# Kernel optimization log

Measured on AMD Instinct MI355X. Metric: run time of the kernel, lower is better.

## Reference

```python
import jax, jax.numpy as jnp
import numpy as np
from jax import lax

B, H, W, C = 8, 128, 128, 192
NUM_HEADS = 4
EPS = 1e-12  # tf.nn.l2_normalize epsilon


def _l2_normalize(x, axis=-1):
    sq = jnp.sum(x * x, axis=axis, keepdims=True)
    return x * lax.rsqrt(jnp.maximum(sq, EPS))


def setup_inputs() -> dict:
    key = jax.random.key(0)
    k1, k2, k3, k4 = jax.random.split(key, 4)
    x = jax.random.normal(k1, (B, H, W, C), dtype=jnp.float32)
    # 1x1 conv -> stored as [C, 3C] matrix
    qkv_w = jax.random.normal(k2, (C, 3 * C), dtype=jnp.float32) * 0.05
    # depthwise 3x3 conv, groups = 3C: HWIO kernel with I=1, O=3C
    dw_w = jax.random.normal(k3, (3, 3, 1, 3 * C), dtype=jnp.float32) * 0.05
    # 1x1 projection conv -> [C, C]
    proj_w = jax.random.normal(k4, (C, C), dtype=jnp.float32) * 0.05
    temperature = jnp.ones((NUM_HEADS, 1, 1), dtype=jnp.float32)
    return {"x": x, "qkv_w": qkv_w, "dw_w": dw_w, "proj_w": proj_w,
            "temperature": temperature}


def reference(x, qkv_w, dw_w, proj_w, temperature):
    b, h, w, c = x.shape
    heads = NUM_HEADS
    c_head = c // heads
    hw = h * w

    # 1x1 conv (no bias)
    qkv = jnp.einsum('bhwc,cd->bhwd', x, qkv_w)  # [b,h,w,3c]
    # depthwise 3x3 conv, SAME padding, groups = 3c
    qkv = lax.conv_general_dilated(
        qkv, dw_w, window_strides=(1, 1), padding='SAME',
        dimension_numbers=('NHWC', 'HWIO', 'NHWC'),
        feature_group_count=3 * c)

    q, k, v = jnp.split(qkv, 3, axis=-1)  # each [b,h,w,c]
    # faithful raw row-major reshape as in the TF code
    q = q.reshape(b, heads, c_head, hw)
    k = k.reshape(b, heads, c_head, hw)
    v = v.reshape(b, heads, c_head, hw)

    q = _l2_normalize(q, axis=-1)
    k = _l2_normalize(k, axis=-1)

    # channel-wise (transposed) attention: [b,heads,c_head,c_head]
    attn = jnp.einsum('bncs,bnds->bncd', q, k)
    attn = attn * temperature[None]  # temperature: [heads,1,1]
    attn = jax.nn.softmax(attn, axis=-1)

    out = jnp.einsum('bncd,bnds->bncs', attn, v)  # [b,heads,c_head,hw]
    out = out.reshape(b, h, w, c)
    out = jnp.einsum('bhwc,cd->bhwd', out, proj_w)  # 1x1 projection
    return out
```

## Files before the change

kernel.cpp:

```cpp
#include <hip/hip_runtime.h>
#include <math.h>

#define HWP 16384
#define CIN 192
#define C3  576
#define CH  48
#define NHD 4
#define NS  32
#define PBF 3145728
#define KG  192

typedef unsigned short u16;
typedef __attribute__((ext_vector_type(8))) short bf16x8;
typedef __attribute__((ext_vector_type(4))) float f32x4;

__device__ __forceinline__ u16 f2bf(float f) {
  unsigned int u = __builtin_bit_cast(unsigned int, f);
  u = (u + 0x7FFFu + ((u >> 16) & 1u)) >> 16;
  return (u16)u;
}
__device__ __forceinline__ float bflo(unsigned int u) {
  return __builtin_bit_cast(float, u << 16);
}
__device__ __forceinline__ float bfhi(unsigned int u) {
  return __builtin_bit_cast(float, u & 0xFFFF0000u);
}
__device__ __forceinline__ unsigned pk2(float a, float b) {
  return (unsigned)f2bf(a) | ((unsigned)f2bf(b) << 16);
}

__device__ __forceinline__ void gload16(const u16* g, u16* l) {
  __builtin_amdgcn_global_load_lds(
      (const __attribute__((address_space(1))) void*)g,
      (__attribute__((address_space(3))) void*)l, 16, 0, 0);
}

__global__ __launch_bounds__(256) void convert_x_k(
    const float* __restrict__ in, u16* __restrict__ out) {
  size_t base = ((size_t)blockIdx.x * 256 + threadIdx.x) * 8;
  float4 a = *(const float4*)&in[base];
  float4 b = *(const float4*)&in[base + 4];
  uint4 o;
  o.x = pk2(a.x, a.y); o.y = pk2(a.z, a.w);
  o.z = pk2(b.x, b.y); o.w = pk2(b.z, b.w);
  *(uint4*)&out[base] = o;
}

__global__ __launch_bounds__(256) void convert_w_k(
    const float* __restrict__ qkvW, const float* __restrict__ projW,
    u16* __restrict__ qkvWT, u16* __restrict__ projWT) {
  int idx = blockIdx.x * 256 + threadIdx.x;
  if (idx < C3 * CIN) {
    int n = idx / CIN, k = idx % CIN;
    qkvWT[idx] = f2bf(qkvW[(size_t)k * C3 + n]);
  } else {
    int i2 = idx - C3 * CIN;
    if (i2 < CIN * CIN) {
      int n = i2 / CIN, k = i2 % CIN;
      projWT[i2] = f2bf(projW[(size_t)k * CIN + n]);
    }
  }
}

template <bool C_BF16>
__global__ __launch_bounds__(256) void gemm1(
    const u16* __restrict__ A, const u16* __restrict__ BT, void* __restrict__ Cv,
    int N) {
  __shared__ __align__(16) u16 As[128 * KG];
  __shared__ __align__(16) u16 Bs[64 * KG];
  const int t = threadIdx.x;
  const int lane = t & 63, wave = t >> 6;
  const int nT = N >> 6;
  const int nwg = gridDim.x;
  const int bid = blockIdx.x;
  const int q = nwg >> 3, r = nwg & 7;
  const int xcd = bid & 7, idx = bid >> 3;
  const int swz = (xcd < r) ? (xcd * (q + 1) + idx)
                            : (r * (q + 1) + (xcd - r) * q + idx);
  const int m0 = (swz / nT) * 128, n0 = (swz % nT) * 64;
  const int wm = (wave >> 1) * 64, wn = (wave & 1) * 32;
  const int wbase = wave * 64;

#pragma unroll
  for (int i = 0; i < 12; ++i) {
    int slot = i * 256 + t;
    int row = slot / 24, c = slot % 24;
    int g = (c & ~7) | ((c & 7) ^ (row & 7));
    gload16(A + (size_t)(m0 + row) * KG + g * 8, As + (size_t)(i * 256 + wbase) * 8);
  }
#pragma unroll
  for (int i = 0; i < 6; ++i) {
    int slot = i * 256 + t;
    int row = slot / 24, c = slot % 24;
    int g = (c & ~7) | ((c & 7) ^ (row & 7));
    gload16(BT + (size_t)(n0 + row) * KG + g * 8, Bs + (size_t)(i * 256 + wbase) * 8);
  }
  __syncthreads();

  f32x4 acc[4][2];
#pragma unroll
  for (int mi = 0; mi < 4; ++mi)
#pragma unroll
    for (int ni = 0; ni < 2; ++ni) acc[mi][ni] = (f32x4){0.f, 0.f, 0.f, 0.f};

  const int lrow = lane & 15;
  const int lg16 = (lane >> 4) * 16;
#pragma unroll
  for (int kk = 0; kk < 6; ++kk) {
    const int colb = kk * 64 + lg16;
    bf16x8 a[4], b[2];
#pragma unroll
    for (int mi = 0; mi < 4; ++mi) {
      int row = wm + mi * 16 + lrow;
      a[mi] = *(const bf16x8*)((char*)As + row * 384 + (colb ^ ((row & 7) << 4)));
    }
#pragma unroll
    for (int ni = 0; ni < 2; ++ni) {
      int row = wn + ni * 16 + lrow;
      b[ni] = *(const bf16x8*)((char*)Bs + row * 384 + (colb ^ ((row & 7) << 4)));
    }
#pragma unroll
    for (int mi = 0; mi < 4; ++mi)
#pragma unroll
      for (int ni = 0; ni < 2; ++ni)
        acc[mi][ni] = __builtin_amdgcn_mfma_f32_16x16x32_bf16(a[mi], b[ni], acc[mi][ni], 0, 0, 0);
  }

  const int crow = (lane >> 4) * 4, ccol = lane & 15;
#pragma unroll
  for (int mi = 0; mi < 4; ++mi)
#pragma unroll
    for (int ni = 0; ni < 2; ++ni)
#pragma unroll
      for (int rr = 0; rr < 4; ++rr) {
        size_t off = (size_t)(m0 + wm + mi * 16 + crow + rr) * N + n0 + wn + ni * 16 + ccol;
        if (C_BF16) ((u16*)Cv)[off] = f2bf(acc[mi][ni][rr]);
        else        ((float*)Cv)[off] = acc[mi][ni][rr];
      }
}

__global__ __launch_bounds__(192) void dwconv_k(
    const u16* __restrict__ pre, const float* __restrict__ dwW,
    u16* __restrict__ qb, u16* __restrict__ kb, u16* __restrict__ vb,
    float* __restrict__ psum, int b0) {
  __shared__ __align__(16) u16 lds[2400 * 8];
  const int t = threadIdx.x;
  const int tile = blockIdx.x, sel = blockIdx.y, brel = blockIdx.z;
  const int h0 = (tile >> 4) * 8, w0 = (tile & 15) * 8;
  const int cg = t % 24, tw = t / 24;
  const int c = sel * 192 + cg * 8;

  float wgt[9][8];
#pragma unroll
  for (int tap = 0; tap < 9; ++tap) {
    float4 a = *(const float4*)&dwW[(size_t)tap * C3 + c];
    float4 b = *(const float4*)&dwW[(size_t)tap * C3 + c + 4];
    wgt[tap][0] = a.x; wgt[tap][1] = a.y; wgt[tap][2] = a.z; wgt[tap][3] = a.w;
    wgt[tap][4] = b.x; wgt[tap][5] = b.y; wgt[tap][6] = b.z; wgt[tap][7] = b.w;
  }

  const u16* src = pre + (size_t)brel * HWP * C3;
#pragma unroll
  for (int r = 0; r < 13; ++r) {
    int slot = t + r * 192;
    if (slot < 2400) {
      int pix = r * 8 + tw;
      int py = pix / 10, px = pix % 10;
      int gh = h0 - 1 + py, gw = w0 - 1 + px;
      uint4 v = make_uint4(0, 0, 0, 0);
      if ((unsigned)gh < 128u && (unsigned)gw < 128u)
        v = *(const uint4*)&src[(size_t)((gh << 7) + gw) * C3 + c];
      *(uint4*)&lds[slot * 8] = v;
    }
  }
  __syncthreads();

  float ssum[8] = {};
  u16* dstb = (sel == 0 ? qb : sel == 1 ? kb : vb) + (size_t)brel * PBF;
#pragma unroll
  for (int r = 0; r < 8; ++r) {
    float acc[8] = {};
#pragma unroll
    for (int dy = 0; dy < 3; ++dy)
#pragma unroll
      for (int dx = 0; dx < 3; ++dx) {
        uint4 v = *(const uint4*)&lds[(((r + dy) * 10 + tw + dx) * 24 + cg) * 8];
        const float* wg = wgt[dy * 3 + dx];
        acc[0] += bflo(v.x) * wg[0]; acc[1] += bfhi(v.x) * wg[1];
        acc[2] += bflo(v.y) * wg[2]; acc[3] += bfhi(v.y) * wg[3];
        acc[4] += bflo(v.z) * wg[4]; acc[5] += bfhi(v.z) * wg[5];
        acc[6] += bflo(v.w) * wg[6]; acc[7] += bfhi(v.w) * wg[7];
      }
    uint4 o;
    o.x = pk2(acc[0], acc[1]); o.y = pk2(acc[2], acc[3]);
    o.z = pk2(acc[4], acc[5]); o.w = pk2(acc[6], acc[7]);
    *(uint4*)&dstb[(size_t)(((h0 + r) << 7) + w0 + tw) * CIN + cg * 8] = o;
    if (sel < 2) {
#pragma unroll
      for (int i = 0; i < 8; ++i) ssum[i] += acc[i] * acc[i];
    }
  }

  if (sel < 2) {
    __syncthreads();
    float* fl = (float*)lds;
#pragma unroll
    for (int i = 0; i < 8; ++i) fl[tw * 192 + cg * 8 + i] = ssum[i];
    __syncthreads();
    float s = 0.f;
#pragma unroll
    for (int tw2 = 0; tw2 < 8; ++tw2) s += fl[tw2 * 192 + t];
    psum[(((size_t)sel * 8 + (b0 + brel)) * 192 + t) * 256 + tile] = s;
  }
}

__global__ __launch_bounds__(192) void rownorm2_k(
    const float* __restrict__ psum, float* __restrict__ rq, float* __restrict__ rk,
    int b0) {
  int sel = blockIdx.x, brel = blockIdx.y;
  int b = b0 + brel;
  int t = threadIdx.x;
  const float* p = psum + (((size_t)sel * 8 + b) * 192 + t) * 256;
  float s = 0.f;
#pragma unroll 4
  for (int i = 0; i < 256; i += 4) {
    float4 v = *(const float4*)&p[i];
    s += v.x + v.y + v.z + v.w;
  }
  (sel ? rk : rq)[b * CIN + t] = rsqrtf(fmaxf(s, 1e-12f));
}

__global__ __launch_bounds__(64) void qk_mfma_k(
    const u16* __restrict__ qbuf, const u16* __restrict__ kbuf,
    float* __restrict__ partial, int b0) {
  int sc = blockIdx.x, n = blockIdx.y, brel = blockIdx.z;
  int b = b0 + brel;
  const int lane = threadIdx.x;
  const u16* qp = qbuf + (size_t)brel * PBF + (size_t)n * CH * HWP;
  const u16* kp = kbuf + (size_t)brel * PBF + (size_t)n * CH * HWP;
  const int lrow = lane & 15;
  const int lko = (lane >> 4) * 8;
  f32x4 acc[3][3];
#pragma unroll
  for (int mi = 0; mi < 3; ++mi)
#pragma unroll
    for (int nj = 0; nj < 3; ++nj) acc[mi][nj] = (f32x4){0.f, 0.f, 0.f, 0.f};

  const int sBeg = sc * 512;
#pragma unroll 4
  for (int kk = 0; kk < 16; ++kk) {
    const int s0 = sBeg + kk * 32 + lko;
    bf16x8 a[3], bb[3];
#pragma unroll
    for (int mi = 0; mi < 3; ++mi)
      a[mi] = *(const bf16x8*)&qp[(size_t)(mi * 16 + lrow) * HWP + s0];
#pragma unroll
    for (int nj = 0; nj < 3; ++nj)
      bb[nj] = *(const bf16x8*)&kp[(size_t)(nj * 16 + lrow) * HWP + s0];
#pragma unroll
    for (int mi = 0; mi < 3; ++mi)
#pragma unroll
      for (int nj = 0; nj < 3; ++nj)
        acc[mi][nj] = __builtin_amdgcn_mfma_f32_16x16x32_bf16(a[mi], bb[nj], acc[mi][nj], 0, 0, 0);
  }

  const int crow = (lane >> 4) * 4, ccol = lane & 15;
  float* pout = partial + (((size_t)b * NHD + n) * NS + sc) * CH * CH;
#pragma unroll
  for (int mi = 0; mi < 3; ++mi)
#pragma unroll
    for (int nj = 0; nj < 3; ++nj)
#pragma unroll
      for (int rr = 0; rr < 4; ++rr)
        pout[(size_t)(mi * 16 + crow + rr) * CH + nj * 16 + ccol] = acc[mi][nj][rr];
}

__global__ __launch_bounds__(64) void softmax_k(
    const float* __restrict__ partial, const float* __restrict__ rq, const float* __restrict__ rk,
    const float* __restrict__ temp, float* __restrict__ attn, int b0) {
  int i = blockIdx.x % CH;
  int n = (blockIdx.x / CH) % NHD;
  int brel = blockIdx.x / (CH * NHD);
  int b = b0 + brel;
  int j = threadIdx.x;
  float logit = -INFINITY;
  if (j < CH) {
    float s = 0.f;
#pragma unroll 8
    for (int sc = 0; sc < NS; ++sc)
      s += partial[((((size_t)b * NHD + n) * NS + sc) * CH + i) * CH + j];
    logit = s * rq[b * CIN + n * CH + i] * rk[b * CIN + n * CH + j] * temp[n];
  }
  float m = logit;
#pragma unroll
  for (int o = 32; o > 0; o >>= 1) m = fmaxf(m, __shfl_xor(m, o));
  float e = (j < CH) ? expf(logit - m) : 0.f;
  float sum = e;
#pragma unroll
  for (int o = 32; o > 0; o >>= 1) sum += __shfl_xor(sum, o);
  if (j < CH) attn[(((size_t)b * NHD + n) * CH + i) * CH + j] = e / sum;
}

__global__ __launch_bounds__(256) void av_k(
    const float* __restrict__ attn, const u16* __restrict__ vbuf,
    u16* __restrict__ obuf, int b0) {
  int st = blockIdx.x, n = blockIdx.y, brel = blockIdx.z;
  int b = b0 + brel;
  __shared__ float as_[CH * CH];
  int t = threadIdx.x;
  const float* ap = attn + ((size_t)b * NHD + n) * CH * CH;
#pragma unroll
  for (int r = 0; r < 9; ++r) as_[t + r * 256] = ap[t + r * 256];
  __syncthreads();
  int s = st * 512 + t * 2;
  const u16* vp = vbuf + (size_t)brel * PBF + (size_t)n * CH * HWP;
  float2 acc[CH];
#pragma unroll
  for (int d = 0; d < CH; ++d) { acc[d].x = 0.f; acc[d].y = 0.f; }
#pragma unroll 4
  for (int j4 = 0; j4 < 12; ++j4) {
    unsigned int u0 = *(const unsigned int*)&vp[(size_t)(j4 * 4 + 0) * HWP + s];
    unsigned int u1 = *(const unsigned int*)&vp[(size_t)(j4 * 4 + 1) * HWP + s];
    unsigned int u2 = *(const unsigned int*)&vp[(size_t)(j4 * 4 + 2) * HWP + s];
    unsigned int u3 = *(const unsigned int*)&vp[(size_t)(j4 * 4 + 3) * HWP + s];
    float2 v0 = make_float2(bflo(u0), bfhi(u0));
    float2 v1 = make_float2(bflo(u1), bfhi(u1));
    float2 v2 = make_float2(bflo(u2), bfhi(u2));
    float2 v3 = make_float2(bflo(u3), bfhi(u3));
#pragma unroll
    for (int d = 0; d < CH; ++d) {
      float4 a4 = *(const float4*)&as_[d * CH + j4 * 4];
      acc[d].x += a4.x * v0.x + a4.y * v1.x + a4.z * v2.x + a4.w * v3.x;
      acc[d].y += a4.x * v0.y + a4.y * v1.y + a4.z * v2.y + a4.w * v3.y;
    }
  }
  u16* op = obuf + (size_t)brel * PBF + (size_t)n * CH * HWP;
#pragma unroll
  for (int d = 0; d < CH; ++d) {
    ushort2 o; o.x = f2bf(acc[d].x); o.y = f2bf(acc[d].y);
    *(ushort2*)&op[(size_t)d * HWP + s] = o;
  }
}

extern "C" void kernel_launch(void* const* d_in, const int* in_sizes, int n_in,
                              void* d_out, int out_size, void* d_ws, size_t ws_size,
                              hipStream_t stream) {
  const float* x      = (const float*)d_in[0];
  const float* qkv_w  = (const float*)d_in[1];
  const float* dw_w   = (const float*)d_in[2];
  const float* proj_w = (const float*)d_in[3];
  const float* temp   = (const float*)d_in[4];
  float* out = (float*)d_out;

  float* rq      = (float*)d_ws;
  float* rk      = rq + 8 * CIN;
  float* attn    = rk + 8 * CIN;
  float* partial = attn + 8 * NHD * CH * CH;
  float* psum    = partial + (size_t)8 * NHD * NS * CH * CH;
  u16* qkvwT  = (u16*)(psum + (size_t)2 * 8 * 192 * 256);
  u16* projwT = qkvwT + (size_t)C3 * CIN;
  u16* xbf    = projwT + (size_t)CIN * CIN;
  char* bufbase = (char*)(xbf + (size_t)8 * HWP * CIN);
  size_t off = (size_t)(bufbase - (char*)d_ws);
  off = (off + 255) & ~(size_t)255;

  const size_t perBatchBytes = (size_t)HWP * C3 * 2 + 4 * (size_t)PBF * 2;
  size_t avail = ws_size > off ? ws_size - off : 0;
  int nb = (int)(avail / perBatchBytes);
  if (nb < 1) nb = 1;
  if (nb > 8) nb = 8;

  u16* qkv_pre = (u16*)((char*)d_ws + off);
  u16* qbuf = qkv_pre + (size_t)nb * HWP * C3;
  u16* kbuf = qbuf + (size_t)nb * PBF;
  u16* vbuf = kbuf + (size_t)nb * PBF;
  u16* obuf = vbuf + (size_t)nb * PBF;

  convert_x_k<<<dim3((8 * HWP * CIN) / 2048), 256, 0, stream>>>(x, xbf);
  convert_w_k<<<dim3((C3 * CIN + CIN * CIN + 255) / 256), 256, 0, stream>>>(
      qkv_w, proj_w, qkvwT, projwT);

  for (int b0 = 0; b0 < 8; b0 += nb) {
    int nbc = (8 - b0) < nb ? (8 - b0) : nb;
    int M = nbc * HWP;
    gemm1<true><<<dim3((M / 128) * (C3 / 64)), 256, 0, stream>>>(
        xbf + (size_t)b0 * HWP * CIN, qkvwT, qkv_pre, C3);
    dwconv_k<<<dim3(256, 3, nbc), 192, 0, stream>>>(
        qkv_pre, dw_w, qbuf, kbuf, vbuf, psum, b0);
    rownorm2_k<<<dim3(2, nbc), 192, 0, stream>>>(psum, rq, rk, b0);
    qk_mfma_k<<<dim3(NS, NHD, nbc), 64, 0, stream>>>(qbuf, kbuf, partial, b0);
    softmax_k<<<dim3(nbc * NHD * CH), 64, 0, stream>>>(partial, rq, rk, temp, attn, b0);
    av_k<<<dim3(HWP / 512, NHD, nbc), 256, 0, stream>>>(attn, vbuf, obuf, b0);
    gemm1<false><<<dim3((M / 128) * (CIN / 64)), 256, 0, stream>>>(
        obuf, projwT, out + (size_t)b0 * HWP * CIN, CIN);
  }
}
```

Baseline: 382.5 us.

## Make GEMM persistent over M tiles with double-buffered A loads

The one-shot 128x64 GEMM kernel is replaced by one where each workgroup keeps its 64-column B tile resident in LDS and walks eight 64-row A tiles. The next A tile is prefetched into a second LDS buffer while the current one is computed. This cuts repeated B loads and launch and prologue overhead per tile, and overlaps global loads with MFMA work. In exchange the grid has fewer workgroups, each wave does less MFMA work per tile, and a barrier is added every iteration.

```diff
diff --git a/kernel.cpp b/kernel.cpp
--- a/kernel.cpp
+++ b/kernel.cpp
@@ -9,6 +9,7 @@
 #define NS  32
 #define PBF 3145728
 #define KG  192
+#define MT  8
 
 typedef unsigned short u16;
 typedef __attribute__((ext_vector_type(8))) short bf16x8;
@@ -63,31 +64,23 @@
 }
 
 template <bool C_BF16>
-__global__ __launch_bounds__(256) void gemm1(
+__global__ __launch_bounds__(256) void gemm2(
     const u16* __restrict__ A, const u16* __restrict__ BT, void* __restrict__ Cv,
     int N) {
-  __shared__ __align__(16) u16 As[128 * KG];
   __shared__ __align__(16) u16 Bs[64 * KG];
+  __shared__ __align__(16) u16 As[2][64 * KG];
   const int t = threadIdx.x;
   const int lane = t & 63, wave = t >> 6;
   const int nT = N >> 6;
-  const int nwg = gridDim.x;
-  const int bid = blockIdx.x;
+  const int nwg = gridDim.x, bid = blockIdx.x;
   const int q = nwg >> 3, r = nwg & 7;
   const int xcd = bid & 7, idx = bid >> 3;
   const int swz = (xcd < r) ? (xcd * (q + 1) + idx)
                             : (r * (q + 1) + (xcd - r) * q + idx);
-  const int m0 = (swz / nT) * 128, n0 = (swz % nT) * 64;
-  const int wm = (wave >> 1) * 64, wn = (wave & 1) * 32;
+  const int n0 = (swz % nT) * 64;
+  const long mbase = (long)(swz / nT) * MT * 64;
   const int wbase = wave * 64;
 
-#pragma unroll
-  for (int i = 0; i < 12; ++i) {
-    int slot = i * 256 + t;
-    int row = slot / 24, c = slot % 24;
-    int g = (c & ~7) | ((c & 7) ^ (row & 7));
-    gload16(A + (size_t)(m0 + row) * KG + g * 8, As + (size_t)(i * 256 + wbase) * 8);
-  }
 #pragma unroll
   for (int i = 0; i < 6; ++i) {
     int slot = i * 256 + t;
@@ -95,48 +88,69 @@
     int g = (c & ~7) | ((c & 7) ^ (row & 7));
     gload16(BT + (size_t)(n0 + row) * KG + g * 8, Bs + (size_t)(i * 256 + wbase) * 8);
   }
+#pragma unroll
+  for (int i = 0; i < 6; ++i) {
+    int slot = i * 256 + t;
+    int row = slot / 24, c = slot % 24;
+    int g = (c & ~7) | ((c & 7) ^ (row & 7));
+    gload16(A + (size_t)(mbase + row) * KG + g * 8, As[0] + (size_t)(i * 256 + wbase) * 8);
+  }
   __syncthreads();
 
-  f32x4 acc[4][2];
-#pragma unroll
-  for (int mi = 0; mi < 4; ++mi)
-#pragma unroll
-    for (int ni = 0; ni < 2; ++ni) acc[mi][ni] = (f32x4){0.f, 0.f, 0.f, 0.f};
-
-  const int lrow = lane & 15;
-  const int lg16 = (lane >> 4) * 16;
-#pragma unroll
-  for (int kk = 0; kk < 6; ++kk) {
-    const int colb = kk * 64 + lg16;
-    bf16x8 a[4], b[2];
-#pragma unroll
-    for (int mi = 0; mi < 4; ++mi) {
-      int row = wm + mi * 16 + lrow;
-      a[mi] = *(const bf16x8*)((char*)As + row * 384 + (colb ^ ((row & 7) << 4)));
-    }
-#pragma unroll
-    for (int ni = 0; ni < 2; ++ni) {
-      int row = wn + ni * 16 + lrow;
-      b[ni] = *(const bf16x8*)((char*)Bs + row * 384 + (colb ^ ((row & 7) << 4)));
-    }
-#pragma unroll
-    for (int mi = 0; mi < 4; ++mi)
+  const int wm = (wave >> 1) * 32, wn = (wave & 1) * 32;
+  const int lrow = lane & 15, lg16 = (lane >> 4) * 16;
+  const int crow = (lane >> 4) * 4, ccol = lane & 15;
+
+  for (int ti = 0; ti < MT; ++ti) {
+    const int cur = ti & 1;
+    if (ti + 1 < MT) {
+#pragma unroll
+      for (int i = 0; i < 6; ++i) {
+        int slot = i * 256 + t;
+        int row = slot / 24, c = slot % 24;
+        int g = (c & ~7) | ((c & 7) ^ (row & 7));
+        gload16(A + (size_t)(mbase + (ti + 1) * 64 + row) * KG + g * 8,
+                As[cur ^ 1] + (size_t)(i * 256 + wbase) * 8);
+      }
+    }
+    f32x4 acc[2][2];
+#pragma unroll
+    for (int mi = 0; mi < 2; ++mi)
+#pragma unroll
+      for (int ni = 0; ni < 2; ++ni) acc[mi][ni] = (f32x4){0.f, 0.f, 0.f, 0.f};
+#pragma unroll
+    for (int kk = 0; kk < 6; ++kk) {
+      const int colb = kk * 64 + lg16;
+      bf16x8 a[2], b[2];
+#pragma unroll
+      for (int mi = 0; mi < 2; ++mi) {
+        int row = wm + mi * 16 + lrow;
+        a[mi] = *(const bf16x8*)((char*)As[cur] + row * 384 + (colb ^ ((row & 7) << 4)));
+      }
+#pragma unroll
+      for (int ni = 0; ni < 2; ++ni) {
+        int row = wn + ni * 16 + lrow;
+        b[ni] = *(const bf16x8*)((char*)Bs + row * 384 + (colb ^ ((row & 7) << 4)));
+      }
+#pragma unroll
+      for (int mi = 0; mi < 2; ++mi)
+#pragma unroll
+        for (int ni = 0; ni < 2; ++ni)
+          acc[mi][ni] = __builtin_amdgcn_mfma_f32_16x16x32_bf16(a[mi], b[ni], acc[mi][ni], 0, 0, 0);
+    }
+    const long m0 = mbase + (long)ti * 64;
+#pragma unroll
+    for (int mi = 0; mi < 2; ++mi)
 #pragma unroll
       for (int ni = 0; ni < 2; ++ni)
-        acc[mi][ni] = __builtin_amdgcn_mfma_f32_16x16x32_bf16(a[mi], b[ni], acc[mi][ni], 0, 0, 0);
-  }
-
-  const int crow = (lane >> 4) * 4, ccol = lane & 15;
-#pragma unroll
-  for (int mi = 0; mi < 4; ++mi)
-#pragma unroll
-    for (int ni = 0; ni < 2; ++ni)
-#pragma unroll
-      for (int rr = 0; rr < 4; ++rr) {
-        size_t off = (size_t)(m0 + wm + mi * 16 + crow + rr) * N + n0 + wn + ni * 16 + ccol;
-        if (C_BF16) ((u16*)Cv)[off] = f2bf(acc[mi][ni][rr]);
-        else        ((float*)Cv)[off] = acc[mi][ni][rr];
-      }
+#pragma unroll
+        for (int rr = 0; rr < 4; ++rr) {
+          size_t off = (size_t)(m0 + wm + mi * 16 + crow + rr) * N + n0 + wn + ni * 16 + ccol;
+          if (C_BF16) ((u16*)Cv)[off] = f2bf(acc[mi][ni][rr]);
+          else        ((float*)Cv)[off] = acc[mi][ni][rr];
+        }
+    __syncthreads();
+  }
 }
 
 __global__ __launch_bounds__(192) void dwconv_k(
@@ -383,7 +397,8 @@
   for (int b0 = 0; b0 < 8; b0 += nb) {
     int nbc = (8 - b0) < nb ? (8 - b0) : nb;
     int M = nbc * HWP;
-    gemm1<true><<<dim3((M / 128) * (C3 / 64)), 256, 0, stream>>>(
+    int mgroups = (M / 64) / MT;
+    gemm2<true><<<dim3(mgroups * (C3 / 64)), 256, 0, stream>>>(
         xbf + (size_t)b0 * HWP * CIN, qkvwT, qkv_pre, C3);
     dwconv_k<<<dim3(256, 3, nbc), 192, 0, stream>>>(
         qkv_pre, dw_w, qbuf, kbuf, vbuf, psum, b0);
@@ -391,7 +406,7 @@
     qk_mfma_k<<<dim3(NS, NHD, nbc), 64, 0, stream>>>(qbuf, kbuf, partial, b0);
     softmax_k<<<dim3(nbc * NHD * CH), 64, 0, stream>>>(partial, rq, rk, temp, attn, b0);
     av_k<<<dim3(HWP / 512, NHD, nbc), 256, 0, stream>>>(attn, vbuf, obuf, b0);
-    gemm1<false><<<dim3((M / 128) * (CIN / 64)), 256, 0, stream>>>(
+    gemm2<false><<<dim3(mgroups * (CIN / 64)), 256, 0, stream>>>(
         obuf, projwT, out + (size_t)b0 * HWP * CIN, CIN);
   }
 }
```

Result: no change. 386.5 us (+1.0%).
